# Optimization experiments

Measured on AMD Instinct MI355X. Metric: run time of the kernel, lower is better.

Reference implementation:

```python
import jax, jax.numpy as jnp
import numpy as np

PLANE_SIZE = 512
FEATURE_DIM = 8
N_LEVELS = 8
MULTISCALE = [1, 2, 4]
LOG2_PS = 9.0  # log2(plane_size)
N_SAMPLES = 1 << 20


def _build_pyramid(tex):
    # tex: [3, R, R, C] -> (flat [3, T, C], sizes [L], offsets [L]) via 2x2 box-filter mips
    levels = [tex]
    t = tex
    for _ in range(N_LEVELS - 1):
        P, h, w, C = t.shape
        t = t.reshape(P, h // 2, 2, w // 2, 2, C).mean(axis=(2, 4))
        levels.append(t)
    sizes = np.array([l.shape[1] for l in levels], dtype=np.int32)
    offsets = np.array([0] + list(np.cumsum(sizes.astype(np.int64) ** 2)[:-1]), dtype=np.int32)
    flat = jnp.concatenate([l.reshape(l.shape[0], -1, l.shape[-1]) for l in levels], axis=1)
    return flat, jnp.asarray(sizes), jnp.asarray(offsets)


def _bilinear_at_level(flat, sizes, offsets, uv, lvl_idx):
    # flat: [3, T, C]; uv: [3, N, 2] in [0,1]; lvl_idx: [3, N] int32
    szi = sizes[lvl_idx]                      # [3, N]
    sz = szi.astype(uv.dtype)
    px = uv[..., 0] * sz - 0.5                # texel centers at (i+0.5)/sz
    py = uv[..., 1] * sz - 0.5
    x0 = jnp.floor(px)
    y0 = jnp.floor(py)
    fx = (px - x0)[..., None]
    fy = (py - y0)[..., None]
    x0i = jnp.clip(x0.astype(jnp.int32), 0, szi - 1)
    x1i = jnp.clip(x0.astype(jnp.int32) + 1, 0, szi - 1)
    y0i = jnp.clip(y0.astype(jnp.int32), 0, szi - 1)
    y1i = jnp.clip(y0.astype(jnp.int32) + 1, 0, szi - 1)
    base = offsets[lvl_idx]

    def gather(yi, xi):
        idx = base + yi * szi + xi            # [3, N]
        return jax.vmap(lambda t, i: t[i])(flat, idx)  # [3, N, C]

    v00 = gather(y0i, x0i)
    v01 = gather(y0i, x1i)
    v10 = gather(y1i, x0i)
    v11 = gather(y1i, x1i)
    top = v00 * (1.0 - fx) + v01 * fx
    bot = v10 * (1.0 - fx) + v11 * fx
    return top * (1.0 - fy) + bot * fy


def _texture(grid, uv, bias):
    # mip-biased trilinear lookup (nvdiffrast linear-mipmap-linear, clamp boundary)
    flat, sizes, offsets = _build_pyramid(grid)
    max_mip = N_LEVELS - 1
    lvl = jnp.clip(bias, 0.0, float(max_mip))
    l0 = jnp.floor(lvl).astype(jnp.int32)
    l1 = jnp.minimum(l0 + 1, max_mip)
    f = (lvl - l0.astype(lvl.dtype))[..., None]
    s0 = _bilinear_at_level(flat, sizes, offsets, uv, l0)
    s1 = _bilinear_at_level(flat, sizes, offsets, uv, l1)
    return s0 * (1.0 - f) + s1 * f            # [3, N, C]


def _forward(x, level, grids):
    n = x.shape[0]
    uv = jnp.stack([x[:, [1, 2]], x[:, [0, 2]], x[:, [0, 1]]], axis=0)  # [3, N, 2]
    lvl = jnp.broadcast_to(level[:, 0][None, :], (3, n))                # [3, N]
    outs = []
    for s, g in enumerate(grids):
        enc = _texture(g, uv, lvl + LOG2_PS + float(s))                 # [3, N, C]
        outs.append(jnp.transpose(enc, (1, 0, 2)).reshape(n, 3 * FEATURE_DIM))
    return jnp.concatenate(outs, axis=-1)     # [N, 3*C*n_scales]


def setup_inputs() -> dict:
    key = jax.random.key(0)
    ks = jax.random.split(key, 5)
    x = jax.random.uniform(ks[0], (N_SAMPLES, 3), dtype=jnp.float32)
    # per-sample LOD so that bias = level + log2(plane_size) + scale spans the mip pyramid
    level = jax.random.uniform(ks[1], (N_SAMPLES, 1), dtype=jnp.float32) * (N_LEVELS - 1) - LOG2_PS
    inp = {"x": x, "level": level}
    for s, mult in enumerate(MULTISCALE):
        r = PLANE_SIZE * mult
        inp[f"grid{s}"] = jax.random.uniform(ks[2 + s], (3, r, r, FEATURE_DIM), jnp.float32, -0.01, 0.01)
    return inp


def reference(x, level, grid0, grid1, grid2):
    return _forward(x, level, (grid0, grid1, grid2))
```

## Files before the change

### kernel.cpp

```cpp
#include <hip/hip_runtime.h>

#define BLK 256
#define SBLK 192
#define NBIN 4096
#define NB 128


#define T0 0
#define T1 1048560
#define T2 2097072
#define TEX_TOTAL 3145392

__device__ __forceinline__ unsigned bfrne(float x) {
    unsigned u = __float_as_uint(x);
    return (u + 0x7fffu + ((u >> 16) & 1u)) >> 16;
}

__device__ __forceinline__ uint4 pack8(const float o[8]) {
    uint4 q;
    q.x = bfrne(o[0]) | (bfrne(o[1]) << 16);
    q.y = bfrne(o[2]) | (bfrne(o[3]) << 16);
    q.z = bfrne(o[4]) | (bfrne(o[5]) << 16);
    q.w = bfrne(o[6]) | (bfrne(o[7]) << 16);
    return q;
}

__device__ __forceinline__ void dec8(const uint4 q, float o[8]) {
    o[0] = __uint_as_float(q.x << 16);
    o[1] = __uint_as_float(q.x & 0xffff0000u);
    o[2] = __uint_as_float(q.y << 16);
    o[3] = __uint_as_float(q.y & 0xffff0000u);
    o[4] = __uint_as_float(q.z << 16);
    o[5] = __uint_as_float(q.z & 0xffff0000u);
    o[6] = __uint_as_float(q.w << 16);
    o[7] = __uint_as_float(q.w & 0xffff0000u);
}

__device__ __forceinline__ void acc8(const uint4 q, float w, float o[8]) {
    o[0] = fmaf(__uint_as_float(q.x << 16), w, o[0]);
    o[1] = fmaf(__uint_as_float(q.x & 0xffff0000u), w, o[1]);
    o[2] = fmaf(__uint_as_float(q.y << 16), w, o[2]);
    o[3] = fmaf(__uint_as_float(q.y & 0xffff0000u), w, o[3]);
    o[4] = fmaf(__uint_as_float(q.z << 16), w, o[4]);
    o[5] = fmaf(__uint_as_float(q.z & 0xffff0000u), w, o[5]);
    o[6] = fmaf(__uint_as_float(q.w << 16), w, o[6]);
    o[7] = fmaf(__uint_as_float(q.w & 0xffff0000u), w, o[7]);
}

__global__ void __launch_bounds__(BLK) base_build_kernel(
    const float* __restrict__ g0, const float* __restrict__ g1,
    const float* __restrict__ g2, uint4* __restrict__ wsT,
    int bA, int bB, int bC) {
    int j = blockIdx.x * BLK + threadIdx.x;
    if (j >= bC) return;
    if (j < bA) {
        const float4* sp = (const float4*)g0 + (size_t)j * 2;
        float4 a = sp[0], b = sp[1];
        float o[8] = {a.x, a.y, a.z, a.w, b.x, b.y, b.z, b.w};
        wsT[T0 + j] = pack8(o);
    } else if (j < bB) {
        int t = j - bA;
        int p = t >> 18;
        int rem = t & ((1 << 18) - 1);
        int y = rem >> 9;
        int x = rem & 511;
        const float4* sp = (const float4*)g1 + (size_t)p * 1024 * 1024 * 2;
        float o[8] = {0, 0, 0, 0, 0, 0, 0, 0};
#pragma unroll
        for (int dy = 0; dy < 2; ++dy) {
#pragma unroll
            for (int dx = 0; dx < 2; ++dx) {
                size_t idx = ((size_t)(2 * y + dy) * 1024 + (2 * x + dx)) * 2;
                float4 a = sp[idx], b = sp[idx + 1];
                o[0] += a.x; o[1] += a.y; o[2] += a.z; o[3] += a.w;
                o[4] += b.x; o[5] += b.y; o[6] += b.z; o[7] += b.w;
            }
        }
#pragma unroll
        for (int c = 0; c < 8; ++c) o[c] *= 0.25f;
        wsT[T1 + t] = pack8(o);
    } else {
        int t = j - bB;
        int p = t >> 18;
        int rem = t & ((1 << 18) - 1);
        int y = rem >> 9;
        int x = rem & 511;
        const float4* sp = (const float4*)g2 + (size_t)p * 2048 * 2048 * 2;
        float o[8] = {0, 0, 0, 0, 0, 0, 0, 0};
#pragma unroll
        for (int dy = 0; dy < 4; ++dy) {
#pragma unroll
            for (int dx = 0; dx < 4; ++dx) {
                size_t idx = ((size_t)(4 * y + dy) * 2048 + (4 * x + dx)) * 2;
                float4 a = sp[idx], b = sp[idx + 1];
                o[0] += a.x; o[1] += a.y; o[2] += a.z; o[3] += a.w;
                o[4] += b.x; o[5] += b.y; o[6] += b.z; o[7] += b.w;
            }
        }
#pragma unroll
        for (int c = 0; c < 8; ++c) o[c] *= 0.0625f;
        wsT[T2 + t] = pack8(o);
    }
}

__global__ void __launch_bounds__(BLK) down2b_kernel(
    uint4* __restrict__ wsT,
    int srcA, int dstA, int lszA, int bA,
    int srcB, int dstB, int lszB, int bB,
    int srcC, int dstC, int lszC, int bC) {
    int j = blockIdx.x * BLK + threadIdx.x;
    if (j >= bC) return;
    int src, dst, lsz;
    if (j < bA) {
        src = srcA; dst = dstA; lsz = lszA;
    } else if (j < bB) {
        src = srcB; dst = dstB; lsz = lszB; j -= bA;
    } else {
        src = srcC; dst = dstC; lsz = lszC; j -= bB;
    }
    int sz = 1 << lsz;
    int p = j >> (2 * lsz);
    int rem = j & (sz * sz - 1);
    int y = rem >> lsz;
    int x = rem & (sz - 1);
    int S = sz << 1;
    const uint4* sp = wsT + src + (size_t)p * S * S;
    size_t i00 = (size_t)(2 * y) * S + 2 * x;
    float d0[8], d1[8], d2[8], d3[8];
    dec8(sp[i00], d0);
    dec8(sp[i00 + 1], d1);
    dec8(sp[i00 + S], d2);
    dec8(sp[i00 + S + 1], d3);
    float o[8];
#pragma unroll
    for (int c = 0; c < 8; ++c) o[c] = (d0[c] + d1[c] + d2[c] + d3[c]) * 0.25f;
    wsT[dst + (size_t)(p << (2 * lsz)) + rem] = pack8(o);
}

__device__ __forceinline__ unsigned spread3(unsigned v) {
    return (v & 1u) | ((v & 2u) << 2) | ((v & 4u) << 4);
}

__device__ __forceinline__ unsigned mkey(float a, float b, float c, float lev) {
    int il = (int)(lev + 9.0f); il = min(max(il, 0), 7);
    int ia = (int)(a * 8.0f); ia = min(max(ia, 0), 7);
    int ib = (int)(b * 8.0f); ib = min(max(ib, 0), 7);
    int ic = (int)(c * 8.0f); ic = min(max(ic, 0), 7);
    unsigned m = (spread3((unsigned)ia) << 2) | (spread3((unsigned)ib) << 1) | spread3((unsigned)ic);
    return (m << 3) | (unsigned)il;
}

__global__ void __launch_bounds__(BLK) hist_kernel(
    const float* __restrict__ x, const float* __restrict__ level,
    unsigned* __restrict__ counts, int n, int chunk) {
    __shared__ unsigned h[NBIN];
    for (int b = threadIdx.x; b < NBIN; b += BLK) h[b] = 0;
    __syncthreads();
    int blk = blockIdx.x;
    int lo = blk * chunk, hi = min(lo + chunk, n);
    for (int i = lo + (int)threadIdx.x; i < hi; i += BLK) {
        unsigned key = mkey(x[3 * i], x[3 * i + 1], x[3 * i + 2], level[i]);
        atomicAdd(&h[key], 1u);
    }
    __syncthreads();
    for (int b = threadIdx.x; b < NBIN; b += BLK)
        counts[(size_t)b * NB + blk] = h[b];
}

__global__ void __launch_bounds__(NB) scanA_kernel(
    unsigned* __restrict__ counts, unsigned* __restrict__ binTotal) {
    __shared__ unsigned tmp[NB];
    int bin = blockIdx.x, t = threadIdx.x;
    unsigned v = counts[(size_t)bin * NB + t];
    tmp[t] = v;
    __syncthreads();
    for (int d = 1; d < NB; d <<= 1) {
        unsigned u = (t >= d) ? tmp[t - d] : 0u;
        __syncthreads();
        tmp[t] += u;
        __syncthreads();
    }
    counts[(size_t)bin * NB + t] = tmp[t] - v;
    if (t == NB - 1) binTotal[bin] = tmp[t];
}

__global__ void __launch_bounds__(1024) scanB_kernel(
    const unsigned* __restrict__ binTotal, unsigned* __restrict__ binBase) {
    __shared__ unsigned tmp[1024];
    int t = threadIdx.x;
    unsigned v0 = binTotal[4 * t];
    unsigned v1 = binTotal[4 * t + 1];
    unsigned v2 = binTotal[4 * t + 2];
    unsigned v3 = binTotal[4 * t + 3];
    unsigned sum = v0 + v1 + v2 + v3;
    tmp[t] = sum;
    __syncthreads();
    for (int d = 1; d < 1024; d <<= 1) {
        unsigned u = (t >= d) ? tmp[t - d] : 0u;
        __syncthreads();
        tmp[t] += u;
        __syncthreads();
    }
    unsigned base = tmp[t] - sum;
    binBase[4 * t] = base;
    binBase[4 * t + 1] = base + v0;
    binBase[4 * t + 2] = base + v0 + v1;
    binBase[4 * t + 3] = base + v0 + v1 + v2;
}

__global__ void __launch_bounds__(BLK) scatter_kernel(
    const float* __restrict__ x, const float* __restrict__ level,
    const unsigned* __restrict__ prefix, const unsigned* __restrict__ binBase,
    float4* __restrict__ xs, unsigned* __restrict__ perm, int n, int chunk) {
    __shared__ unsigned h[NBIN];
    for (int b = threadIdx.x; b < NBIN; b += BLK) h[b] = 0;
    __syncthreads();
    int blk = blockIdx.x;
    int lo = blk * chunk, hi = min(lo + chunk, n);
    for (int i = lo + (int)threadIdx.x; i < hi; i += BLK) {
        float a = x[3 * i], b = x[3 * i + 1], c = x[3 * i + 2];
        float lv = level[i];
        unsigned key = mkey(a, b, c, lv);
        unsigned r = atomicAdd(&h[key], 1u);
        unsigned pos = binBase[key] + prefix[(size_t)key * NB + blk] + r;
        xs[pos] = make_float4(a, b, c, lv);
        perm[pos] = (unsigned)i;
    }
}

__device__ __forceinline__ void addr4(const uint4* __restrict__ t, int sz,
                                      float u, float v,
                                      const uint4** a, float* w) {
    float fsz = (float)sz;
    float px = u * fsz - 0.5f;
    float py = v * fsz - 0.5f;
    float x0f = floorf(px), y0f = floorf(py);
    float fx = px - x0f, fy = py - y0f;
    int xi = (int)x0f, yi = (int)y0f;
    int m = sz - 1;
    int x0 = min(max(xi, 0), m);
    int x1 = min(max(xi + 1, 0), m);
    int y0 = min(max(yi, 0), m);
    int y1 = min(max(yi + 1, 0), m);
    const uint4* r0 = t + (size_t)y0 * sz;
    const uint4* r1 = t + (size_t)y1 * sz;
    a[0] = r0 + x0;
    a[1] = r0 + x1;
    a[2] = r1 + x0;
    a[3] = r1 + x1;
    w[0] = (1.0f - fx) * (1.0f - fy);
    w[1] = fx * (1.0f - fy);
    w[2] = (1.0f - fx) * fy;
    w[3] = fx * fy;
}

__global__ void __launch_bounds__(SBLK) tex_sample_kernel(
    const float4* __restrict__ xs, const unsigned* __restrict__ perm,
    const uint4* __restrict__ wsT, float* __restrict__ out, int n) {
    int nblk = gridDim.x;
    int cpx = nblk >> 3;
    int bid = blockIdx.x;
    int bswz = (bid & 7) * cpx + (bid >> 3);
    int lane = threadIdx.x & 63;
    int s = threadIdx.x >> 6;
    int j = bswz * 64 + lane;
    if (j >= n) return;
    float4 xl = xs[j];
    float xv0 = xl.x, xv1 = xl.y, xv2 = xl.z, lev = xl.w;
    unsigned oi = perm[j];

    const int WSS_[3] = {T0, T1, T2};
    const int OFFMIN_[3] = {0, 1048576, 5242880};

    const int R = 512 << s;
    float bias = lev + 9.0f + (float)s;
    float lvl = fminf(fmaxf(bias, 0.0f), 7.0f);
    float l0f = floorf(lvl);
    int l0 = (int)l0f;
    int l1 = min(l0 + 1, 7);
    float f = lvl - l0f;
    int sz0 = R >> l0;
    int sz1 = R >> l1;
    int off0 = ((R * R - sz0 * sz0) * 4) / 3;
    int off1 = ((R * R - sz1 * sz1) * 4) / 3;
    const uint4* base0 = wsT + WSS_[s] + (size_t)3 * (off0 - OFFMIN_[s]);
    const uint4* base1 = wsT + WSS_[s] + (size_t)3 * (off1 - OFFMIN_[s]);

    const uint4* ap[24];
    float w[6][4];
#pragma unroll
    for (int p = 0; p < 3; ++p) {
        float u = (p == 0) ? xv1 : xv0;
        float v = (p == 2) ? xv1 : xv2;
        addr4(base0 + (size_t)p * (sz0 * sz0), sz0, u, v, &ap[8 * p], w[2 * p]);
        addr4(base1 + (size_t)p * (sz1 * sz1), sz1, u, v, &ap[8 * p + 4], w[2 * p + 1]);
    }
    uint4 q[24];
#pragma unroll
    for (int t = 0; t < 24; ++t) q[t] = *ap[t];

    float* op = out + (size_t)oi * 72 + s * 24;
    float omf = 1.0f - f;
#pragma unroll
    for (int p = 0; p < 3; ++p) {
        float a[8] = {0, 0, 0, 0, 0, 0, 0, 0};
        float b[8] = {0, 0, 0, 0, 0, 0, 0, 0};
#pragma unroll
        for (int t = 0; t < 4; ++t) acc8(q[8 * p + t], w[2 * p][t], a);
#pragma unroll
        for (int t = 0; t < 4; ++t) acc8(q[8 * p + 4 + t], w[2 * p + 1][t], b);
        float4 r0, r1;
        r0.x = a[0] * omf + b[0] * f;
        r0.y = a[1] * omf + b[1] * f;
        r0.z = a[2] * omf + b[2] * f;
        r0.w = a[3] * omf + b[3] * f;
        r1.x = a[4] * omf + b[4] * f;
        r1.y = a[5] * omf + b[5] * f;
        r1.z = a[6] * omf + b[6] * f;
        r1.w = a[7] * omf + b[7] * f;
        float4* o4 = (float4*)(op + p * 8);
        o4[0] = r0;
        o4[1] = r1;
    }
}

extern "C" void kernel_launch(void* const* d_in, const int* in_sizes, int n_in,
                              void* d_out, int out_size, void* d_ws, size_t ws_size,
                              hipStream_t stream) {
    const float* x = (const float*)d_in[0];
    const float* level = (const float*)d_in[1];
    const float* g0 = (const float*)d_in[2];
    const float* g1 = (const float*)d_in[3];
    const float* g2 = (const float*)d_in[4];
    float* out = (float*)d_out;
    uint4* wsT = (uint4*)d_ws;
    int n = in_sizes[0] / 3;

    float4* xs = (float4*)(wsT + TEX_TOTAL);
    unsigned* perm = (unsigned*)(xs + n);
    unsigned* counts = perm + n;
    unsigned* binTotal = counts + (size_t)NBIN * NB;
    unsigned* binBase = binTotal + NBIN;

    auto lvlOff = [](int s, int l) -> int {
        const int WSS[3] = {T0, T1, T2};
        const int OFFMIN[3] = {0, 1048576, 5242880};
        int R = 512 << s;
        int sz = R >> l;
        int off = ((R * R - sz * sz) * 4) / 3;
        return WSS[s] + 3 * (off - OFFMIN[s]);
    };

    {
        int bA = 3 * 512 * 512;
        int bB = bA * 2;
        int bC = bA * 3;
        base_build_kernel<<<(bC + BLK - 1) / BLK, BLK, 0, stream>>>(
            g0, g1, g2, wsT, bA, bB, bC);
    }
    for (int l = 1; l <= 7; ++l) {
        int szA = 512 >> l;
        int bA = 3 * szA * szA;
        int srcA = lvlOff(0, l - 1), dstA = lvlOff(0, l), lszA = 9 - l;
        int bB = bA, srcB = 0, dstB = 0, lszB = 0;
        int bC = bA, srcC = 0, dstC = 0, lszC = 0;
        if (l >= 2) {
            int szB = 1024 >> l;
            bB = bA + 3 * szB * szB;
            srcB = lvlOff(1, l - 1); dstB = lvlOff(1, l); lszB = 10 - l;
            bC = bB;
        }
        if (l >= 3) {
            int szC = 2048 >> l;
            bC = bB + 3 * szC * szC;
            srcC = lvlOff(2, l - 1); dstC = lvlOff(2, l); lszC = 11 - l;
        }
        down2b_kernel<<<(bC + BLK - 1) / BLK, BLK, 0, stream>>>(
            wsT, srcA, dstA, lszA, bA, srcB, dstB, lszB, bB, srcC, dstC, lszC, bC);
    }

    int chunk = (n + NB - 1) / NB;
    hist_kernel<<<NB, BLK, 0, stream>>>(x, level, counts, n, chunk);
    scanA_kernel<<<NBIN, NB, 0, stream>>>(counts, binTotal);
    scanB_kernel<<<1, 1024, 0, stream>>>(binTotal, binBase);
    scatter_kernel<<<NB, BLK, 0, stream>>>(x, level, counts, binBase, xs, perm, n, chunk);

    int nblk = (n + 63) / 64;
    nblk = (nblk + 7) & ~7;
    tex_sample_kernel<<<nblk, SBLK, 0, stream>>>(xs, perm, wsT, out, n);
}
```

Before: 445.3 us.

## Fuse histogram into base build, widen histogram blocks, stage outputs via LDS

Merges the histogram pass into the base-level pyramid build kernel as extra blocks, which removes one launch and lets the two run concurrently. Doubles the number of histogram and scatter blocks, which also doubles the width of the per-bin scan. In the sampling kernel, results are staged in shared memory so that each scale's 24-float slice per sample is written with cooperatively distributed float4 stores instead of per-thread strided stores. This adds a block barrier and LDS traffic in the sampling kernel.

```diff
diff --git a/kernel.cpp b/kernel.cpp
--- a/kernel.cpp
+++ b/kernel.cpp
@@ -3,7 +3,7 @@
 #define BLK 256
 #define SBLK 192
 #define NBIN 4096
-#define NB 128
+#define NB 256
 
 
 #define T0 0
@@ -47,10 +47,40 @@
     o[7] = fmaf(__uint_as_float(q.w & 0xffff0000u), w, o[7]);
 }
 
-__global__ void __launch_bounds__(BLK) base_build_kernel(
+__device__ __forceinline__ unsigned spread3(unsigned v) {
+    return (v & 1u) | ((v & 2u) << 2) | ((v & 4u) << 4);
+}
+
+__device__ __forceinline__ unsigned mkey(float a, float b, float c, float lev) {
+    int il = (int)(lev + 9.0f); il = min(max(il, 0), 7);
+    int ia = (int)(a * 8.0f); ia = min(max(ia, 0), 7);
+    int ib = (int)(b * 8.0f); ib = min(max(ib, 0), 7);
+    int ic = (int)(c * 8.0f); ic = min(max(ic, 0), 7);
+    unsigned m = (spread3((unsigned)ia) << 2) | (spread3((unsigned)ib) << 1) | spread3((unsigned)ic);
+    return (m << 3) | (unsigned)il;
+}
+
+__global__ void __launch_bounds__(BLK) base_hist_kernel(
     const float* __restrict__ g0, const float* __restrict__ g1,
     const float* __restrict__ g2, uint4* __restrict__ wsT,
-    int bA, int bB, int bC) {
+    const float* __restrict__ x, const float* __restrict__ level,
+    unsigned* __restrict__ counts,
+    int bA, int bB, int bC, int bBase, int n, int chunk) {
+    if ((int)blockIdx.x >= bBase) {
+        __shared__ unsigned h[NBIN];
+        for (int b = threadIdx.x; b < NBIN; b += BLK) h[b] = 0;
+        __syncthreads();
+        int blk = blockIdx.x - bBase;
+        int lo = blk * chunk, hi = min(lo + chunk, n);
+        for (int i = lo + (int)threadIdx.x; i < hi; i += BLK) {
+            unsigned key = mkey(x[3 * i], x[3 * i + 1], x[3 * i + 2], level[i]);
+            atomicAdd(&h[key], 1u);
+        }
+        __syncthreads();
+        for (int b = threadIdx.x; b < NBIN; b += BLK)
+            counts[(size_t)b * NB + blk] = h[b];
+        return;
+    }
     int j = blockIdx.x * BLK + threadIdx.x;
     if (j >= bC) return;
     if (j < bA) {
@@ -63,14 +93,14 @@
         int p = t >> 18;
         int rem = t & ((1 << 18) - 1);
         int y = rem >> 9;
-        int x = rem & 511;
+        int x2 = rem & 511;
         const float4* sp = (const float4*)g1 + (size_t)p * 1024 * 1024 * 2;
         float o[8] = {0, 0, 0, 0, 0, 0, 0, 0};
 #pragma unroll
         for (int dy = 0; dy < 2; ++dy) {
 #pragma unroll
             for (int dx = 0; dx < 2; ++dx) {
-                size_t idx = ((size_t)(2 * y + dy) * 1024 + (2 * x + dx)) * 2;
+                size_t idx = ((size_t)(2 * y + dy) * 1024 + (2 * x2 + dx)) * 2;
                 float4 a = sp[idx], b = sp[idx + 1];
                 o[0] += a.x; o[1] += a.y; o[2] += a.z; o[3] += a.w;
                 o[4] += b.x; o[5] += b.y; o[6] += b.z; o[7] += b.w;
@@ -84,14 +114,14 @@
         int p = t >> 18;
         int rem = t & ((1 << 18) - 1);
         int y = rem >> 9;
-        int x = rem & 511;
+        int x2 = rem & 511;
         const float4* sp = (const float4*)g2 + (size_t)p * 2048 * 2048 * 2;
         float o[8] = {0, 0, 0, 0, 0, 0, 0, 0};
 #pragma unroll
         for (int dy = 0; dy < 4; ++dy) {
 #pragma unroll
             for (int dx = 0; dx < 4; ++dx) {
-                size_t idx = ((size_t)(4 * y + dy) * 2048 + (4 * x + dx)) * 2;
+                size_t idx = ((size_t)(4 * y + dy) * 2048 + (4 * x2 + dx)) * 2;
                 float4 a = sp[idx], b = sp[idx + 1];
                 o[0] += a.x; o[1] += a.y; o[2] += a.z; o[3] += a.w;
                 o[4] += b.x; o[5] += b.y; o[6] += b.z; o[7] += b.w;
@@ -135,36 +165,6 @@
 #pragma unroll
     for (int c = 0; c < 8; ++c) o[c] = (d0[c] + d1[c] + d2[c] + d3[c]) * 0.25f;
     wsT[dst + (size_t)(p << (2 * lsz)) + rem] = pack8(o);
-}
-
-__device__ __forceinline__ unsigned spread3(unsigned v) {
-    return (v & 1u) | ((v & 2u) << 2) | ((v & 4u) << 4);
-}
-
-__device__ __forceinline__ unsigned mkey(float a, float b, float c, float lev) {
-    int il = (int)(lev + 9.0f); il = min(max(il, 0), 7);
-    int ia = (int)(a * 8.0f); ia = min(max(ia, 0), 7);
-    int ib = (int)(b * 8.0f); ib = min(max(ib, 0), 7);
-    int ic = (int)(c * 8.0f); ic = min(max(ic, 0), 7);
-    unsigned m = (spread3((unsigned)ia) << 2) | (spread3((unsigned)ib) << 1) | spread3((unsigned)ic);
-    return (m << 3) | (unsigned)il;
-}
-
-__global__ void __launch_bounds__(BLK) hist_kernel(
-    const float* __restrict__ x, const float* __restrict__ level,
-    unsigned* __restrict__ counts, int n, int chunk) {
-    __shared__ unsigned h[NBIN];
-    for (int b = threadIdx.x; b < NBIN; b += BLK) h[b] = 0;
-    __syncthreads();
-    int blk = blockIdx.x;
-    int lo = blk * chunk, hi = min(lo + chunk, n);
-    for (int i = lo + (int)threadIdx.x; i < hi; i += BLK) {
-        unsigned key = mkey(x[3 * i], x[3 * i + 1], x[3 * i + 2], level[i]);
-        atomicAdd(&h[key], 1u);
-    }
-    __syncthreads();
-    for (int b = threadIdx.x; b < NBIN; b += BLK)
-        counts[(size_t)b * NB + blk] = h[b];
 }
 
 __global__ void __launch_bounds__(NB) scanA_kernel(
@@ -257,70 +257,83 @@
 __global__ void __launch_bounds__(SBLK) tex_sample_kernel(
     const float4* __restrict__ xs, const unsigned* __restrict__ perm,
     const uint4* __restrict__ wsT, float* __restrict__ out, int n) {
+    __shared__ float so[3][64][25];
+    __shared__ unsigned soi[64];
     int nblk = gridDim.x;
     int cpx = nblk >> 3;
     int bid = blockIdx.x;
     int bswz = (bid & 7) * cpx + (bid >> 3);
     int lane = threadIdx.x & 63;
     int s = threadIdx.x >> 6;
-    int j = bswz * 64 + lane;
-    if (j >= n) return;
-    float4 xl = xs[j];
-    float xv0 = xl.x, xv1 = xl.y, xv2 = xl.z, lev = xl.w;
-    unsigned oi = perm[j];
-
-    const int WSS_[3] = {T0, T1, T2};
-    const int OFFMIN_[3] = {0, 1048576, 5242880};
-
-    const int R = 512 << s;
-    float bias = lev + 9.0f + (float)s;
-    float lvl = fminf(fmaxf(bias, 0.0f), 7.0f);
-    float l0f = floorf(lvl);
-    int l0 = (int)l0f;
-    int l1 = min(l0 + 1, 7);
-    float f = lvl - l0f;
-    int sz0 = R >> l0;
-    int sz1 = R >> l1;
-    int off0 = ((R * R - sz0 * sz0) * 4) / 3;
-    int off1 = ((R * R - sz1 * sz1) * 4) / 3;
-    const uint4* base0 = wsT + WSS_[s] + (size_t)3 * (off0 - OFFMIN_[s]);
-    const uint4* base1 = wsT + WSS_[s] + (size_t)3 * (off1 - OFFMIN_[s]);
-
-    const uint4* ap[24];
-    float w[6][4];
-#pragma unroll
-    for (int p = 0; p < 3; ++p) {
-        float u = (p == 0) ? xv1 : xv0;
-        float v = (p == 2) ? xv1 : xv2;
-        addr4(base0 + (size_t)p * (sz0 * sz0), sz0, u, v, &ap[8 * p], w[2 * p]);
-        addr4(base1 + (size_t)p * (sz1 * sz1), sz1, u, v, &ap[8 * p + 4], w[2 * p + 1]);
-    }
-    uint4 q[24];
-#pragma unroll
-    for (int t = 0; t < 24; ++t) q[t] = *ap[t];
-
-    float* op = out + (size_t)oi * 72 + s * 24;
-    float omf = 1.0f - f;
-#pragma unroll
-    for (int p = 0; p < 3; ++p) {
-        float a[8] = {0, 0, 0, 0, 0, 0, 0, 0};
-        float b[8] = {0, 0, 0, 0, 0, 0, 0, 0};
-#pragma unroll
-        for (int t = 0; t < 4; ++t) acc8(q[8 * p + t], w[2 * p][t], a);
-#pragma unroll
-        for (int t = 0; t < 4; ++t) acc8(q[8 * p + 4 + t], w[2 * p + 1][t], b);
-        float4 r0, r1;
-        r0.x = a[0] * omf + b[0] * f;
-        r0.y = a[1] * omf + b[1] * f;
-        r0.z = a[2] * omf + b[2] * f;
-        r0.w = a[3] * omf + b[3] * f;
-        r1.x = a[4] * omf + b[4] * f;
-        r1.y = a[5] * omf + b[5] * f;
-        r1.z = a[6] * omf + b[6] * f;
-        r1.w = a[7] * omf + b[7] * f;
-        float4* o4 = (float4*)(op + p * 8);
-        o4[0] = r0;
-        o4[1] = r1;
+    int base = bswz * 64;
+    int j = base + lane;
+    bool valid = j < n;
+
+    if (valid) {
+        float4 xl = xs[j];
+        float xv0 = xl.x, xv1 = xl.y, xv2 = xl.z, lev = xl.w;
+        if (s == 0) soi[lane] = perm[j];
+
+        const int WSS_[3] = {T0, T1, T2};
+        const int OFFMIN_[3] = {0, 1048576, 5242880};
+
+        const int R = 512 << s;
+        float bias = lev + 9.0f + (float)s;
+        float lvl = fminf(fmaxf(bias, 0.0f), 7.0f);
+        float l0f = floorf(lvl);
+        int l0 = (int)l0f;
+        int l1 = min(l0 + 1, 7);
+        float f = lvl - l0f;
+        int sz0 = R >> l0;
+        int sz1 = R >> l1;
+        int off0 = ((R * R - sz0 * sz0) * 4) / 3;
+        int off1 = ((R * R - sz1 * sz1) * 4) / 3;
+        const uint4* base0 = wsT + WSS_[s] + (size_t)3 * (off0 - OFFMIN_[s]);
+        const uint4* base1 = wsT + WSS_[s] + (size_t)3 * (off1 - OFFMIN_[s]);
+
+        const uint4* ap[24];
+        float w[6][4];
+#pragma unroll
+        for (int p = 0; p < 3; ++p) {
+            float u = (p == 0) ? xv1 : xv0;
+            float v = (p == 2) ? xv1 : xv2;
+            addr4(base0 + (size_t)p * (sz0 * sz0), sz0, u, v, &ap[8 * p], w[2 * p]);
+            addr4(base1 + (size_t)p * (sz1 * sz1), sz1, u, v, &ap[8 * p + 4], w[2 * p + 1]);
+        }
+        uint4 q[24];
+#pragma unroll
+        for (int t = 0; t < 24; ++t) q[t] = *ap[t];
+
+        float omf = 1.0f - f;
+#pragma unroll
+        for (int p = 0; p < 3; ++p) {
+            float a[8] = {0, 0, 0, 0, 0, 0, 0, 0};
+            float b[8] = {0, 0, 0, 0, 0, 0, 0, 0};
+#pragma unroll
+            for (int t = 0; t < 4; ++t) acc8(q[8 * p + t], w[2 * p][t], a);
+#pragma unroll
+            for (int t = 0; t < 4; ++t) acc8(q[8 * p + 4 + t], w[2 * p + 1][t], b);
+#pragma unroll
+            for (int c = 0; c < 8; ++c)
+                so[s][lane][8 * p + c] = a[c] * omf + b[c] * f;
+        }
+    }
+    __syncthreads();
+    if (valid) {
+#pragma unroll
+        for (int k = 0; k < 6; ++k) {
+            int e = k * 64 + lane;
+            int sample = (e * 10923) >> 16;
+            int word = e - 6 * sample;
+            if (base + sample < n) {
+                float4 v;
+                v.x = so[s][sample][word * 4 + 0];
+                v.y = so[s][sample][word * 4 + 1];
+                v.z = so[s][sample][word * 4 + 2];
+                v.w = so[s][sample][word * 4 + 3];
+                *(float4*)(out + (size_t)soi[sample] * 72 + s * 24 + word * 4) = v;
+            }
+        }
     }
 }
 
@@ -351,12 +364,15 @@
         return WSS[s] + 3 * (off - OFFMIN[s]);
     };
 
+    int chunk = (n + NB - 1) / NB;
+
     {
         int bA = 3 * 512 * 512;
         int bB = bA * 2;
         int bC = bA * 3;
-        base_build_kernel<<<(bC + BLK - 1) / BLK, BLK, 0, stream>>>(
-            g0, g1, g2, wsT, bA, bB, bC);
+        int bBase = (bC + BLK - 1) / BLK;
+        base_hist_kernel<<<bBase + NB, BLK, 0, stream>>>(
+            g0, g1, g2, wsT, x, level, counts, bA, bB, bC, bBase, n, chunk);
     }
     for (int l = 1; l <= 7; ++l) {
         int szA = 512 >> l;
@@ -379,8 +395,6 @@
             wsT, srcA, dstA, lszA, bA, srcB, dstB, lszB, bB, srcC, dstC, lszC, bC);
     }
 
-    int chunk = (n + NB - 1) / NB;
-    hist_kernel<<<NB, BLK, 0, stream>>>(x, level, counts, n, chunk);
     scanA_kernel<<<NBIN, NB, 0, stream>>>(counts, binTotal);
     scanB_kernel<<<1, 1024, 0, stream>>>(binTotal, binBase);
     scatter_kernel<<<NB, BLK, 0, stream>>>(x, level, counts, binBase, xs, perm, n, chunk);
```

New measurement: 412.6 us. 1.08x faster.
